# Kernel optimization log

Hardware: AMD Instinct MI355X
Metric: run time of the kernel (lower is better)

The kernel has to match this reference:

```python
import jax, jax.numpy as jnp
import numpy as np

HIDDEN = 4096
NUM_HEADS = 32
GROUP_NUM = 8
HEAD_DIM = HIDDEN // NUM_HEADS


def setup_inputs() -> dict:
    key = jax.random.key(0)
    ks = jax.random.split(key, 9)
    s = 0.02
    kv_dim = GROUP_NUM * HEAD_DIM
    return {
        "hidden_state": jax.random.normal(ks[0], (1, 2048, HIDDEN), dtype=jnp.float32),
        "wq": jax.random.normal(ks[1], (HIDDEN, HIDDEN), dtype=jnp.float32) * s,
        "bq": jnp.zeros((HIDDEN,), dtype=jnp.float32),
        "wk": jax.random.normal(ks[2], (HIDDEN, kv_dim), dtype=jnp.float32) * s,
        "bk": jnp.zeros((kv_dim,), dtype=jnp.float32),
        "wv": jax.random.normal(ks[3], (HIDDEN, kv_dim), dtype=jnp.float32) * s,
        "bv": jnp.zeros((kv_dim,), dtype=jnp.float32),
        "wo": jax.random.normal(ks[4], (HIDDEN, HIDDEN), dtype=jnp.float32) * s,
        "bo": jnp.zeros((HIDDEN,), dtype=jnp.float32),
    }


def reference(hidden_state, wq, bq, wk, bk, wv, bv, wo, bo):
    B, S, _ = hidden_state.shape
    q = hidden_state @ wq + bq                      # [B,S,H*D]
    k = hidden_state @ wk + bk                      # [B,S,G*D]
    v = hidden_state @ wv + bv                      # [B,S,G*D]

    q = q.reshape(B, S, NUM_HEADS, HEAD_DIM).transpose(0, 2, 1, 3)   # [B,H,S,D]
    k = k.reshape(B, S, GROUP_NUM, HEAD_DIM).transpose(0, 2, 1, 3)   # [B,G,S,D]
    v = v.reshape(B, S, GROUP_NUM, HEAD_DIM).transpose(0, 2, 1, 3)
    # broadcast KV groups to all heads (repeat each group heads_per_group times)
    rep = NUM_HEADS // GROUP_NUM
    k = jnp.repeat(k, rep, axis=1)                  # [B,H,S,D]
    v = jnp.repeat(v, rep, axis=1)

    scale = 1.0 / jnp.sqrt(jnp.float32(HEAD_DIM))
    scores = jnp.einsum("bhqd,bhkd->bhqk", q, k) * scale  # [B,H,S,S]
    probs = jax.nn.softmax(scores, axis=-1)
    out = jnp.einsum("bhqk,bhkd->bhqd", probs, v)         # [B,H,S,D]
    # faithful to original: transpose(-1,-2) then view (NOT a standard head merge)
    out = jnp.swapaxes(out, -1, -2).reshape(B, -1, HEAD_DIM * NUM_HEADS)  # [B,S,H*D]
    return out @ wo + bo
```

## Files before the change

kernel.cpp:

```cpp
#include <hip/hip_runtime.h>
#include <stdint.h>

#define HIDDEN 4096
#define SEQ    2048
#define NHEADS 32
#define HDIM   128
#define KVDIM  1024

typedef __attribute__((ext_vector_type(8))) short short8;
typedef __attribute__((ext_vector_type(4))) unsigned short ushort4v;
typedef __attribute__((ext_vector_type(4))) float f32x4;
typedef __attribute__((ext_vector_type(16))) float f32x16;
typedef __attribute__((ext_vector_type(4))) float float4v;
typedef __attribute__((ext_vector_type(4))) int int4v;

__device__ __forceinline__ unsigned short f2bf(float f) {
    union { float f; unsigned u; } v; v.f = f;
    unsigned r = v.u + 0x7FFFu + ((v.u >> 16) & 1u);
    return (unsigned short)(r >> 16);
}

__device__ __forceinline__ float fexp2(float x) {
#if __has_builtin(__builtin_amdgcn_exp2f)
    return __builtin_amdgcn_exp2f(x);
#else
    return exp2f(x);
#endif
}

__global__ void cast_bf16_kernel(const float* __restrict__ in,
                                 unsigned short* __restrict__ out, int n4) {
    int i = blockIdx.x * blockDim.x + threadIdx.x;
    if (i >= n4) return;
    float4v v = *(const float4v*)(in + (size_t)i * 4);
    ushort4v o;
    o.x = f2bf(v.x); o.y = f2bf(v.y); o.z = f2bf(v.z); o.w = f2bf(v.w);
    *(ushort4v*)(out + (size_t)i * 4) = o;
}

__global__ void transpose_cast_all_kernel(const float* __restrict__ wq,
                                          const float* __restrict__ wk,
                                          const float* __restrict__ wv,
                                          const float* __restrict__ wo,
                                          unsigned short* __restrict__ wqkvt,
                                          unsigned short* __restrict__ wot) {
    __shared__ float tile[64][65];
    int cx = blockIdx.x;
    const float* src; unsigned short* dst; int C; int cxl;
    if (cx < 64)      { src = wq; dst = wqkvt; C = HIDDEN; cxl = cx; }
    else if (cx < 80) { src = wk; dst = wqkvt + (size_t)4096 * HIDDEN; C = KVDIM; cxl = cx - 64; }
    else if (cx < 96) { src = wv; dst = wqkvt + (size_t)5120 * HIDDEN; C = KVDIM; cxl = cx - 80; }
    else              { src = wo; dst = wot;   C = HIDDEN; cxl = cx - 96; }
    const int R = HIDDEN;
    int r0 = blockIdx.y << 6, c0 = cxl << 6;
    int t = threadIdx.x;
    int lr = t >> 4, lc = (t & 15) << 2;
#pragma unroll
    for (int i = 0; i < 4; i++) {
        int r = lr + i * 16;
        float4v v = *(const float4v*)(src + (size_t)(r0 + r) * C + c0 + lc);
        tile[r][lc] = v.x; tile[r][lc + 1] = v.y;
        tile[r][lc + 2] = v.z; tile[r][lc + 3] = v.w;
    }
    __syncthreads();
#pragma unroll
    for (int i = 0; i < 4; i++) {
        int c = lr + i * 16;
        ushort4v o;
        o.x = f2bf(tile[lc][c]);     o.y = f2bf(tile[lc + 1][c]);
        o.z = f2bf(tile[lc + 2][c]); o.w = f2bf(tile[lc + 3][c]);
        *(ushort4v*)(dst + (size_t)(c0 + c) * R + r0 + lc) = o;
    }
}

__device__ __forceinline__ void gload_lds16(const void* g, void* l) {
    __builtin_amdgcn_global_load_lds(
        (const __attribute__((address_space(1))) void*)g,
        (__attribute__((address_space(3))) void*)l, 16, 0, 0);
}

template <int MODE>
__global__ __launch_bounds__(512, 1)
void gemm8_kernel(const unsigned short* __restrict__ A,
                  const unsigned short* __restrict__ Bt,
                  const float* __restrict__ b0,
                  const float* __restrict__ b1,
                  const float* __restrict__ b2,
                  unsigned short* __restrict__ Qo,
                  unsigned short* __restrict__ Ko,
                  unsigned short* __restrict__ Vto,
                  float* __restrict__ Of,
                  float qscale) {
    const int K = HIDDEN;
    __shared__ __align__(16) char lds[3 * 49152];

    int t = threadIdx.x;
    int w = t >> 6, l = t & 63;
    int fr = l & 15, fq = l >> 4;
    int wm = w >> 2, wn = w & 3;

    int nwg = gridDim.x * gridDim.y;
    int orig = blockIdx.y * gridDim.x + blockIdx.x;
    int cpx = nwg >> 3;
    int swz = (orig & 7) * cpx + (orig >> 3);
    int bx = swz % gridDim.x, by = swz / gridDim.x;
    int mbase = by * 128, nbase = bx * 256;

    int rA = t >> 3;
    int lch = (t & 7) ^ (rA & 7);
    const unsigned short* pA0 = A + (size_t)(mbase + rA) * K + lch * 8;
    const unsigned short* pA1 = pA0 + (size_t)64 * K;
    const unsigned short* pB0 = Bt + (size_t)(nbase + rA) * K + lch * 8;
    const unsigned short* pB1 = pB0 + (size_t)64 * K;
    const unsigned short* pB2 = pB0 + (size_t)128 * K;
    const unsigned short* pB3 = pB0 + (size_t)192 * K;
    int wo16 = w * 1024;

    int offA[4][2], offB[4][2];
#pragma unroll
    for (int m = 0; m < 4; m++) {
        int row = wm * 64 + m * 16 + fr;
#pragma unroll
        for (int kk = 0; kk < 2; kk++)
            offA[m][kk] = row * 128 + (((kk << 2) + fq) ^ (row & 7)) * 16;
    }
#pragma unroll
    for (int n = 0; n < 4; n++) {
        int row = wn * 64 + n * 16 + fr;
#pragma unroll
        for (int kk = 0; kk < 2; kk++)
            offB[n][kk] = 16384 + row * 128 + (((kk << 2) + fq) ^ (row & 7)) * 16;
    }

    f32x4 acc[4][4];
    f32x4 z = {0.f, 0.f, 0.f, 0.f};
#pragma unroll
    for (int m = 0; m < 4; m++)
#pragma unroll
        for (int n = 0; n < 4; n++) acc[m][n] = z;

    const int NT = K / 64;

#define STAGE6(bufbase, ts)                                            \
    {                                                                  \
        size_t ko = (size_t)(ts) * 64;                                 \
        char* lb = lds + (bufbase);                                    \
        gload_lds16(pA0 + ko, lb + wo16);                              \
        gload_lds16(pA1 + ko, lb + 8192 + wo16);                       \
        gload_lds16(pB0 + ko, lb + 16384 + wo16);                      \
        gload_lds16(pB1 + ko, lb + 24576 + wo16);                      \
        gload_lds16(pB2 + ko, lb + 32768 + wo16);                      \
        gload_lds16(pB3 + ko, lb + 40960 + wo16);                      \
    }

    STAGE6(0, 0);
    STAGE6(49152, 1);

    int cb = 0;
    for (int tt = 0; tt < NT; ++tt) {
        if (tt + 1 < NT) asm volatile("s_waitcnt vmcnt(6)" ::: "memory");
        else             asm volatile("s_waitcnt vmcnt(0)" ::: "memory");
        __builtin_amdgcn_s_barrier();
        __builtin_amdgcn_sched_barrier(0);
        if (tt + 2 < NT) {
            int sb = (cb == 0) ? 2 : cb - 1;
            STAGE6(sb * 49152, tt + 2);
        }
        const char* base = lds + cb * 49152;
#pragma unroll
        for (int kk = 0; kk < 2; kk++) {
            short8 af[4], bf[4];
#pragma unroll
            for (int m = 0; m < 4; m++) af[m] = *(const short8*)(base + offA[m][kk]);
#pragma unroll
            for (int n = 0; n < 4; n++) bf[n] = *(const short8*)(base + offB[n][kk]);
            __builtin_amdgcn_s_setprio(1);
#pragma unroll
            for (int m = 0; m < 4; m++)
#pragma unroll
                for (int n = 0; n < 4; n++)
                    acc[m][n] = __builtin_amdgcn_mfma_f32_16x16x32_bf16(af[m], bf[n], acc[m][n], 0, 0, 0);
            __builtin_amdgcn_s_setprio(0);
        }
        cb = (cb == 2) ? 0 : cb + 1;
    }
#undef STAGE6

    if (MODE == 1) {
        if (nbase < 4096) {
#pragma unroll
            for (int n = 0; n < 4; n++) {
                int col = nbase + wn * 64 + n * 16 + fr;
                float bb = b0[col];
#pragma unroll
                for (int m = 0; m < 4; m++) {
                    int row = mbase + wm * 64 + m * 16 + fq * 4;
                    unsigned short* cp = Qo + (size_t)row * HIDDEN + col;
#pragma unroll
                    for (int r = 0; r < 4; r++)
                        cp[(size_t)r * HIDDEN] = f2bf((acc[m][n][r] + bb) * qscale);
                }
            }
        } else if (nbase < 5120) {
#pragma unroll
            for (int n = 0; n < 4; n++) {
                int col = nbase - 4096 + wn * 64 + n * 16 + fr;
                float bb = b1[col];
#pragma unroll
                for (int m = 0; m < 4; m++) {
                    int row = mbase + wm * 64 + m * 16 + fq * 4;
                    unsigned short* cp = Ko + (size_t)row * KVDIM + col;
#pragma unroll
                    for (int r = 0; r < 4; r++)
                        cp[(size_t)r * KVDIM] = f2bf(acc[m][n][r] + bb);
                }
            }
        } else {
#pragma unroll
            for (int n = 0; n < 4; n++) {
                int col = nbase - 5120 + wn * 64 + n * 16 + fr;
                float bb = b2[col];
#pragma unroll
                for (int m = 0; m < 4; m++) {
                    int row = mbase + wm * 64 + m * 16 + fq * 4;
                    ushort4v o;
                    o.x = f2bf(acc[m][n][0] + bb);
                    o.y = f2bf(acc[m][n][1] + bb);
                    o.z = f2bf(acc[m][n][2] + bb);
                    o.w = f2bf(acc[m][n][3] + bb);
                    *(ushort4v*)(Vto + (size_t)col * SEQ + row) = o;
                }
            }
        }
    } else {
#pragma unroll
        for (int n = 0; n < 4; n++) {
            int col = nbase + wn * 64 + n * 16 + fr;
            float bb = b0[col];
#pragma unroll
            for (int m = 0; m < 4; m++) {
                int row = mbase + wm * 64 + m * 16 + fq * 4;
                float* cp = Of + (size_t)row * HIDDEN + col;
#pragma unroll
                for (int r = 0; r < 4; r++)
                    cp[(size_t)r * HIDDEN] = acc[m][n][r] + bb;
            }
        }
    }
}

#define SWZ(off, row) ((off) ^ (((row) & 7) << 4))
__global__ __launch_bounds__(256, 2)
void attn_kernel(const unsigned short* __restrict__ Q,
                 const unsigned short* __restrict__ Kc,
                 const unsigned short* __restrict__ Vt,
                 unsigned short* __restrict__ Mg) {
    __shared__ __align__(16) char Kb[2][64 * 256];
    __shared__ __align__(16) char Vb[2][128 * 128];
    int qb = blockIdx.x, head = blockIdx.y, g = head >> 2;
    int t = threadIdx.x, w = t >> 6, l = t & 63;
    int lq = l & 31, lh = l >> 5;

    short8 qf[8];
    {
        const unsigned short* qp =
            Q + (size_t)(qb * 128 + w * 32 + lq) * HIDDEN + head * HDIM + lh * 8;
#pragma unroll
        for (int kk = 0; kk < 8; kk++) qf[kk] = *(const short8*)(qp + kk * 16);
    }

    f32x16 accO[4];
#pragma unroll
    for (int n = 0; n < 4; n++)
#pragma unroll
        for (int r = 0; r < 16; r++) accO[n][r] = 0.f;
    float Lrun = 0.f;

    int krow = t >> 2; int kcb = (t & 3) * 64;
    int vrow = t >> 1; int vcb = (t & 1) * 64;
    const unsigned short* ksrc = Kc + (size_t)krow * KVDIM + g * HDIM + (t & 3) * 32;
    const unsigned short* vsrc = Vt + (size_t)(g * HDIM + vrow) * SEQ + (t & 1) * 32;
    int kwb = krow * 256 + kcb;
    int vwb = vrow * 128 + vcb;

    const int NT = SEQ / 64;
    short8 kreg[4], vreg[4];
#pragma unroll
    for (int j = 0; j < 4; j++) kreg[j] = *(const short8*)(ksrc + j * 8);
#pragma unroll
    for (int j = 0; j < 4; j++) vreg[j] = *(const short8*)(vsrc + j * 8);
#pragma unroll
    for (int j = 0; j < 4; j++) *(short8*)(Kb[0] + SWZ(kwb + j * 16, krow)) = kreg[j];
#pragma unroll
    for (int j = 0; j < 4; j++) *(short8*)(Vb[0] + SWZ(vwb + j * 16, vrow)) = vreg[j];
#pragma unroll
    for (int j = 0; j < 4; j++) kreg[j] = *(const short8*)(ksrc + (size_t)64 * KVDIM + j * 8);
#pragma unroll
    for (int j = 0; j < 4; j++) vreg[j] = *(const short8*)(vsrc + 64 + j * 8);

    for (int tl = 0; tl < NT; tl++) {
        int b = tl & 1;
        __syncthreads();
        if (tl + 1 < NT) {
#pragma unroll
            for (int j = 0; j < 4; j++) *(short8*)(Kb[b ^ 1] + SWZ(kwb + j * 16, krow)) = kreg[j];
#pragma unroll
            for (int j = 0; j < 4; j++) *(short8*)(Vb[b ^ 1] + SWZ(vwb + j * 16, vrow)) = vreg[j];
            if (tl + 2 < NT) {
                const unsigned short* ks = ksrc + (size_t)(tl + 2) * 64 * KVDIM;
                const unsigned short* vs = vsrc + (tl + 2) * 64;
#pragma unroll
                for (int j = 0; j < 4; j++) kreg[j] = *(const short8*)(ks + j * 8);
#pragma unroll
                for (int j = 0; j < 4; j++) vreg[j] = *(const short8*)(vs + j * 8);
            }
        }
        const char* kb = Kb[b];
        const char* vb = Vb[b];

        f32x16 s0, s1;
#pragma unroll
        for (int r = 0; r < 16; r++) { s0[r] = 0.f; s1[r] = 0.f; }
#pragma unroll
        for (int kk = 0; kk < 8; kk++) {
            int cb2 = kk * 32 + lh * 16;
            short8 kf0 = *(const short8*)(kb + SWZ(lq * 256 + cb2, lq));
            short8 kf1 = *(const short8*)(kb + SWZ((lq + 32) * 256 + cb2, lq));
            s0 = __builtin_amdgcn_mfma_f32_32x32x16_bf16(kf0, qf[kk], s0, 0, 0, 0);
            s1 = __builtin_amdgcn_mfma_f32_32x32x16_bf16(kf1, qf[kk], s1, 0, 0, 0);
        }

        float sum = 0.f;
#pragma unroll
        for (int r = 0; r < 16; r++) { s0[r] = fexp2(s0[r]); sum += s0[r]; }
#pragma unroll
        for (int r = 0; r < 16; r++) { s1[r] = fexp2(s1[r]); sum += s1[r]; }
        sum += __shfl_xor(sum, 32);
        Lrun += sum;

        int W0[8], W1[8];
#pragma unroll
        for (int i = 0; i < 8; i++)
            W0[i] = (int)((unsigned)f2bf(s0[2 * i]) | ((unsigned)f2bf(s0[2 * i + 1]) << 16));
#pragma unroll
        for (int i = 0; i < 8; i++)
            W1[i] = (int)((unsigned)f2bf(s1[2 * i]) | ((unsigned)f2bf(s1[2 * i + 1]) << 16));

        short8 pa[4];
#pragma unroll
        for (int kkp = 0; kkp < 4; kkp++) {
            int k4 = (kkp & 1) * 4;
            int o0 = (kkp < 2) ? W0[k4 + 0] : W1[k4 + 0];
            int o1 = (kkp < 2) ? W0[k4 + 1] : W1[k4 + 1];
            int o2 = (kkp < 2) ? W0[k4 + 2] : W1[k4 + 2];
            int o3 = (kkp < 2) ? W0[k4 + 3] : W1[k4 + 3];
            int Za = lh ? o0 : o2;
            int Zb = lh ? o1 : o3;
            int Xa = __shfl_xor(Za, 32);
            int Xb = __shfl_xor(Zb, 32);
            int4v pw;
            pw.x = lh ? Xa : o0;
            pw.y = lh ? Xb : o1;
            pw.z = lh ? o2 : Xa;
            pw.w = lh ? o3 : Xb;
            pa[kkp] = *(short8*)&pw;
        }

#pragma unroll
        for (int n = 0; n < 4; n++) {
            int row = n * 32 + lq;
#pragma unroll
            for (int kkp = 0; kkp < 4; kkp++) {
                short8 vf = *(const short8*)(vb + SWZ(row * 128 + kkp * 32 + lh * 16, lq));
                accO[n] = __builtin_amdgcn_mfma_f32_32x32x16_bf16(pa[kkp], vf, accO[n], 0, 0, 0);
            }
        }
    }

    float rl[16];
#pragma unroll
    for (int r = 0; r < 16; r++)
        rl[r] = 1.0f / __shfl(Lrun, (r & 3) + 8 * (r >> 2) + 4 * lh);
#pragma unroll
    for (int n = 0; n < 4; n++) {
        int d = n * 32 + lq;
        int mrow = head * 64 + (d >> 1);
#pragma unroll
        for (int g2 = 0; g2 < 4; g2++) {
            int mcol = (d & 1) * SEQ + qb * 128 + w * 32 + 8 * g2 + 4 * lh;
            ushort4v o;
            o.x = f2bf(accO[n][g2 * 4 + 0] * rl[g2 * 4 + 0]);
            o.y = f2bf(accO[n][g2 * 4 + 1] * rl[g2 * 4 + 1]);
            o.z = f2bf(accO[n][g2 * 4 + 2] * rl[g2 * 4 + 2]);
            o.w = f2bf(accO[n][g2 * 4 + 3] * rl[g2 * 4 + 3]);
            *(ushort4v*)(Mg + (size_t)mrow * HIDDEN + mcol) = o;
        }
    }
}

extern "C" void kernel_launch(void* const* d_in, const int* in_sizes, int n_in,
                              void* d_out, int out_size, void* d_ws, size_t ws_size,
                              hipStream_t stream) {
    const float* x  = (const float*)d_in[0];
    const float* wq = (const float*)d_in[1];
    const float* bq = (const float*)d_in[2];
    const float* wk = (const float*)d_in[3];
    const float* bk = (const float*)d_in[4];
    const float* wv = (const float*)d_in[5];
    const float* bv = (const float*)d_in[6];
    const float* wo = (const float*)d_in[7];
    const float* bo = (const float*)d_in[8];

    char* base = (char*)d_ws;
    unsigned short* xb     = (unsigned short*)(base + 0);
    unsigned short* wqkvt  = (unsigned short*)(base + 16777216);
    unsigned short* wot    = (unsigned short*)(base + 67108864);
    unsigned short* qbuf   = (unsigned short*)(base + 100663296);
    unsigned short* kbuf   = (unsigned short*)(base + 117440512);
    unsigned short* vtbuf  = (unsigned short*)(base + 121634816);
    unsigned short* merged = (unsigned short*)(base + 125829120);

    const float QSCALE = 0.08838834764831845f * 1.4426950408889634f;

    cast_bf16_kernel<<<(SEQ * HIDDEN / 4 + 255) / 256, 256, 0, stream>>>(x, xb, SEQ * HIDDEN / 4);
    transpose_cast_all_kernel<<<dim3(160, 64), 256, 0, stream>>>(wq, wk, wv, wo, wqkvt, wot);
    gemm8_kernel<1><<<dim3(6144 / 256, SEQ / 128), 512, 0, stream>>>(
        xb, wqkvt, bq, bk, bv, qbuf, kbuf, vtbuf, nullptr, QSCALE);
    attn_kernel<<<dim3(SEQ / 128, NHEADS), 256, 0, stream>>>(qbuf, kbuf, vtbuf, merged);
    gemm8_kernel<2><<<dim3(HIDDEN / 256, SEQ / 128), 512, 0, stream>>>(
        merged, wot, bo, nullptr, nullptr, nullptr, nullptr, nullptr, (float*)d_out, 1.0f);
}
```

Baseline: 328.8 us.

## Enlarge GEMM tiles to 256x256 with double-buffered LDS pipeline

The projection GEMMs move from 128x256 tiles with a triple-buffered LDS pipeline to 256x256 tiles with double buffering (two 64KB buffers), and each wave now computes an 8x4 grid of MFMA tiles. The larger tile doubles arithmetic per byte loaded from global memory and LDS. The cost is more accumulator registers and fewer workgroups: 192 for the QKV GEMM and 128 for the output GEMM, below the CU count on MI355X. The pipeline now issues the next stage's loads before computing the current one, and each iteration adds a second barrier.

```diff
diff --git a/kernel.cpp b/kernel.cpp
--- a/kernel.cpp
+++ b/kernel.cpp
@@ -80,19 +80,19 @@
 }
 
 template <int MODE>
-__global__ __launch_bounds__(512, 1)
-void gemm8_kernel(const unsigned short* __restrict__ A,
-                  const unsigned short* __restrict__ Bt,
-                  const float* __restrict__ b0,
-                  const float* __restrict__ b1,
-                  const float* __restrict__ b2,
-                  unsigned short* __restrict__ Qo,
-                  unsigned short* __restrict__ Ko,
-                  unsigned short* __restrict__ Vto,
-                  float* __restrict__ Of,
-                  float qscale) {
+__global__ __launch_bounds__(512, 2)
+void gemm256_kernel(const unsigned short* __restrict__ A,
+                    const unsigned short* __restrict__ Bt,
+                    const float* __restrict__ b0,
+                    const float* __restrict__ b1,
+                    const float* __restrict__ b2,
+                    unsigned short* __restrict__ Qo,
+                    unsigned short* __restrict__ Ko,
+                    unsigned short* __restrict__ Vto,
+                    float* __restrict__ Of,
+                    float qscale) {
     const int K = HIDDEN;
-    __shared__ __align__(16) char lds[3 * 49152];
+    __shared__ __align__(16) char lds[2 * 65536];
 
     int t = threadIdx.x;
     int w = t >> 6, l = t & 63;
@@ -104,87 +104,88 @@
     int cpx = nwg >> 3;
     int swz = (orig & 7) * cpx + (orig >> 3);
     int bx = swz % gridDim.x, by = swz / gridDim.x;
-    int mbase = by * 128, nbase = bx * 256;
-
-    int rA = t >> 3;
-    int lch = (t & 7) ^ (rA & 7);
-    const unsigned short* pA0 = A + (size_t)(mbase + rA) * K + lch * 8;
-    const unsigned short* pA1 = pA0 + (size_t)64 * K;
-    const unsigned short* pB0 = Bt + (size_t)(nbase + rA) * K + lch * 8;
-    const unsigned short* pB1 = pB0 + (size_t)64 * K;
-    const unsigned short* pB2 = pB0 + (size_t)128 * K;
-    const unsigned short* pB3 = pB0 + (size_t)192 * K;
-    int wo16 = w * 1024;
-
-    int offA[4][2], offB[4][2];
-#pragma unroll
-    for (int m = 0; m < 4; m++) {
-        int row = wm * 64 + m * 16 + fr;
-#pragma unroll
-        for (int kk = 0; kk < 2; kk++)
-            offA[m][kk] = row * 128 + (((kk << 2) + fq) ^ (row & 7)) * 16;
-    }
-#pragma unroll
-    for (int n = 0; n < 4; n++) {
-        int row = wn * 64 + n * 16 + fr;
-#pragma unroll
-        for (int kk = 0; kk < 2; kk++)
-            offB[n][kk] = 16384 + row * 128 + (((kk << 2) + fq) ^ (row & 7)) * 16;
-    }
-
-    f32x4 acc[4][4];
+    int mbase = by * 256, nbase = bx * 256;
+
+    int rband = t >> 3;
+    int ch = (t & 7) ^ (rband & 7);
+    const unsigned short* pA = A + (size_t)(mbase + rband) * K + ch * 8;
+    const unsigned short* pB = Bt + (size_t)(nbase + rband) * K + ch * 8;
+    int wdst = w * 1024;
+
+    int rbA[8], rbB[4], cko[2];
+#pragma unroll
+    for (int m = 0; m < 8; m++) rbA[m] = (wm * 128 + m * 16 + fr) * 128;
+#pragma unroll
+    for (int n = 0; n < 4; n++) rbB[n] = (wn * 64 + n * 16 + fr) * 128;
+#pragma unroll
+    for (int kk = 0; kk < 2; kk++) cko[kk] = (((kk << 2) + fq) ^ (fr & 7)) * 16;
+
+    f32x4 acc[8][4];
     f32x4 z = {0.f, 0.f, 0.f, 0.f};
 #pragma unroll
-    for (int m = 0; m < 4; m++)
+    for (int m = 0; m < 8; m++)
 #pragma unroll
         for (int n = 0; n < 4; n++) acc[m][n] = z;
 
     const int NT = K / 64;
-
-#define STAGE6(bufbase, ts)                                            \
-    {                                                                  \
-        size_t ko = (size_t)(ts) * 64;                                 \
-        char* lb = lds + (bufbase);                                    \
-        gload_lds16(pA0 + ko, lb + wo16);                              \
-        gload_lds16(pA1 + ko, lb + 8192 + wo16);                       \
-        gload_lds16(pB0 + ko, lb + 16384 + wo16);                      \
-        gload_lds16(pB1 + ko, lb + 24576 + wo16);                      \
-        gload_lds16(pB2 + ko, lb + 32768 + wo16);                      \
-        gload_lds16(pB3 + ko, lb + 40960 + wo16);                      \
-    }
-
-    STAGE6(0, 0);
-    STAGE6(49152, 1);
-
+    const size_t K64 = (size_t)64 * K;
+
+#define STAGE8(bufbase, ts)                                              \
+    {                                                                    \
+        size_t ko = (size_t)(ts) * 64;                                   \
+        char* lb = lds + (bufbase);                                      \
+        gload_lds16(pA + ko,            lb + wdst);                      \
+        gload_lds16(pA + ko + K64,      lb + 8192 + wdst);               \
+        gload_lds16(pA + ko + 2 * K64,  lb + 16384 + wdst);              \
+        gload_lds16(pA + ko + 3 * K64,  lb + 24576 + wdst);              \
+        gload_lds16(pB + ko,            lb + 32768 + wdst);              \
+        gload_lds16(pB + ko + K64,      lb + 40960 + wdst);              \
+        gload_lds16(pB + ko + 2 * K64,  lb + 49152 + wdst);              \
+        gload_lds16(pB + ko + 3 * K64,  lb + 57344 + wdst);              \
+    }
+
+#define COMPUTE(bufbase)                                                          \
+    {                                                                             \
+        const char* _b = lds + (bufbase);                                         \
+        _Pragma("unroll")                                                         \
+        for (int kk = 0; kk < 2; kk++) {                                          \
+            short8 af[8], bf[4];                                                  \
+            _Pragma("unroll")                                                     \
+            for (int m = 0; m < 8; m++)                                           \
+                af[m] = *(const short8*)(_b + rbA[m] + cko[kk]);                  \
+            _Pragma("unroll")                                                     \
+            for (int n = 0; n < 4; n++)                                           \
+                bf[n] = *(const short8*)(_b + 32768 + rbB[n] + cko[kk]);          \
+            __builtin_amdgcn_s_setprio(1);                                        \
+            _Pragma("unroll")                                                     \
+            for (int m = 0; m < 8; m++)                                           \
+                _Pragma("unroll")                                                 \
+                for (int n = 0; n < 4; n++)                                       \
+                    acc[m][n] = __builtin_amdgcn_mfma_f32_16x16x32_bf16(          \
+                        af[m], bf[n], acc[m][n], 0, 0, 0);                        \
+            __builtin_amdgcn_s_setprio(0);                                        \
+        }                                                                         \
+    }
+
+    STAGE8(0, 0);
     int cb = 0;
-    for (int tt = 0; tt < NT; ++tt) {
-        if (tt + 1 < NT) asm volatile("s_waitcnt vmcnt(6)" ::: "memory");
-        else             asm volatile("s_waitcnt vmcnt(0)" ::: "memory");
+    for (int tt = 0; tt < NT - 1; ++tt) {
+        STAGE8((cb ^ 1) * 65536, tt + 1);
+        __builtin_amdgcn_sched_barrier(0);
+        asm volatile("s_waitcnt vmcnt(8)" ::: "memory");
         __builtin_amdgcn_s_barrier();
         __builtin_amdgcn_sched_barrier(0);
-        if (tt + 2 < NT) {
-            int sb = (cb == 0) ? 2 : cb - 1;
-            STAGE6(sb * 49152, tt + 2);
-        }
-        const char* base = lds + cb * 49152;
-#pragma unroll
-        for (int kk = 0; kk < 2; kk++) {
-            short8 af[4], bf[4];
-#pragma unroll
-            for (int m = 0; m < 4; m++) af[m] = *(const short8*)(base + offA[m][kk]);
-#pragma unroll
-            for (int n = 0; n < 4; n++) bf[n] = *(const short8*)(base + offB[n][kk]);
-            __builtin_amdgcn_s_setprio(1);
-#pragma unroll
-            for (int m = 0; m < 4; m++)
-#pragma unroll
-                for (int n = 0; n < 4; n++)
-                    acc[m][n] = __builtin_amdgcn_mfma_f32_16x16x32_bf16(af[m], bf[n], acc[m][n], 0, 0, 0);
-            __builtin_amdgcn_s_setprio(0);
-        }
-        cb = (cb == 2) ? 0 : cb + 1;
-    }
-#undef STAGE6
+        COMPUTE(cb * 65536);
+        __builtin_amdgcn_sched_barrier(0);
+        __builtin_amdgcn_s_barrier();
+        cb ^= 1;
+    }
+    asm volatile("s_waitcnt vmcnt(0)" ::: "memory");
+    __builtin_amdgcn_s_barrier();
+    __builtin_amdgcn_sched_barrier(0);
+    COMPUTE(cb * 65536);
+#undef STAGE8
+#undef COMPUTE
 
     if (MODE == 1) {
         if (nbase < 4096) {
@@ -193,8 +194,8 @@
                 int col = nbase + wn * 64 + n * 16 + fr;
                 float bb = b0[col];
 #pragma unroll
-                for (int m = 0; m < 4; m++) {
-                    int row = mbase + wm * 64 + m * 16 + fq * 4;
+                for (int m = 0; m < 8; m++) {
+                    int row = mbase + wm * 128 + m * 16 + fq * 4;
                     unsigned short* cp = Qo + (size_t)row * HIDDEN + col;
 #pragma unroll
                     for (int r = 0; r < 4; r++)
@@ -207,8 +208,8 @@
                 int col = nbase - 4096 + wn * 64 + n * 16 + fr;
                 float bb = b1[col];
 #pragma unroll
-                for (int m = 0; m < 4; m++) {
-                    int row = mbase + wm * 64 + m * 16 + fq * 4;
+                for (int m = 0; m < 8; m++) {
+                    int row = mbase + wm * 128 + m * 16 + fq * 4;
                     unsigned short* cp = Ko + (size_t)row * KVDIM + col;
 #pragma unroll
                     for (int r = 0; r < 4; r++)
@@ -221,8 +222,8 @@
                 int col = nbase - 5120 + wn * 64 + n * 16 + fr;
                 float bb = b2[col];
 #pragma unroll
-                for (int m = 0; m < 4; m++) {
-                    int row = mbase + wm * 64 + m * 16 + fq * 4;
+                for (int m = 0; m < 8; m++) {
+                    int row = mbase + wm * 128 + m * 16 + fq * 4;
                     ushort4v o;
                     o.x = f2bf(acc[m][n][0] + bb);
                     o.y = f2bf(acc[m][n][1] + bb);
@@ -238,8 +239,8 @@
             int col = nbase + wn * 64 + n * 16 + fr;
             float bb = b0[col];
 #pragma unroll
-            for (int m = 0; m < 4; m++) {
-                int row = mbase + wm * 64 + m * 16 + fq * 4;
+            for (int m = 0; m < 8; m++) {
+                int row = mbase + wm * 128 + m * 16 + fq * 4;
                 float* cp = Of + (size_t)row * HIDDEN + col;
 #pragma unroll
                 for (int r = 0; r < 4; r++)
@@ -424,9 +425,9 @@
 
     cast_bf16_kernel<<<(SEQ * HIDDEN / 4 + 255) / 256, 256, 0, stream>>>(x, xb, SEQ * HIDDEN / 4);
     transpose_cast_all_kernel<<<dim3(160, 64), 256, 0, stream>>>(wq, wk, wv, wo, wqkvt, wot);
-    gemm8_kernel<1><<<dim3(6144 / 256, SEQ / 128), 512, 0, stream>>>(
+    gemm256_kernel<1><<<dim3(6144 / 256, SEQ / 256), 512, 0, stream>>>(
         xb, wqkvt, bq, bk, bv, qbuf, kbuf, vtbuf, nullptr, QSCALE);
     attn_kernel<<<dim3(SEQ / 128, NHEADS), 256, 0, stream>>>(qbuf, kbuf, vtbuf, merged);
-    gemm8_kernel<2><<<dim3(HIDDEN / 256, SEQ / 128), 512, 0, stream>>>(
+    gemm256_kernel<2><<<dim3(HIDDEN / 256, SEQ / 256), 512, 0, stream>>>(
         merged, wot, bo, nullptr, nullptr, nullptr, nullptr, nullptr, (float*)d_out, 1.0f);
 }
```

Result: slower. 363.7 us (+10.6%).
